# Kernel optimization log

Measured on AMD Instinct MI355X. Metric: run time of the kernel, lower is better.

Reference implementation:

```python
import jax, jax.numpy as jnp
import numpy as np

B = 32768
I = 512
H = 512

def setup_inputs() -> dict:
    key = jax.random.key(0)
    ks = jax.random.split(key, 14)
    s_i = 1.0 / np.sqrt(I)
    s_h = 1.0 / np.sqrt(H)
    inp = {
        'x': jax.random.normal(ks[0], (B, I), dtype=jnp.float32),
        'h': jax.random.normal(ks[1], (B, H), dtype=jnp.float32),
        'Wz_w': jax.random.uniform(ks[2], (H, I), jnp.float32, -s_i, s_i),
        'Wz_b': jax.random.uniform(ks[3], (H,), jnp.float32, -s_i, s_i),
        'Wr_w': jax.random.uniform(ks[4], (H, I), jnp.float32, -s_i, s_i),
        'Wr_b': jax.random.uniform(ks[5], (H,), jnp.float32, -s_i, s_i),
        'Wh_w': jax.random.uniform(ks[6], (H, I), jnp.float32, -s_i, s_i),
        'Wh_b': jax.random.uniform(ks[7], (H,), jnp.float32, -s_i, s_i),
        'Uz_w': jax.random.uniform(ks[8], (H, H), jnp.float32, -s_h, s_h),
        'Uz_b': jax.random.uniform(ks[9], (H,), jnp.float32, -s_h, s_h),
        'Ur_w': jax.random.uniform(ks[10], (H, H), jnp.float32, -s_h, s_h),
        'Ur_b': jax.random.uniform(ks[11], (H,), jnp.float32, -s_h, s_h),
        'Uh_w': jax.random.uniform(ks[12], (H, H), jnp.float32, -s_h, s_h),
        'Uh_b': jax.random.uniform(ks[13], (H,), jnp.float32, -s_h, s_h),
    }
    return inp

def reference(x, h, Wz_w, Wz_b, Wr_w, Wr_b, Wh_w, Wh_b, Uz_w, Uz_b, Ur_w, Ur_b, Uh_w, Uh_b):
    # z = sigmoid(Wz x + Uz h); r = sigmoid(Wr x + Ur h)
    z = jax.nn.sigmoid(x @ Wz_w.T + Wz_b + h @ Uz_w.T + Uz_b)
    r = jax.nn.sigmoid(x @ Wr_w.T + Wr_b + h @ Ur_w.T + Ur_b)
    # candidate: tanh(Wh x + Uh (h * r))
    ht = jnp.tanh(x @ Wh_w.T + Wh_b + (h * r) @ Uh_w.T + Uh_b)
    h_next = h + z * (ht - h)
    return (h_next, h_next)
```

## Files before the change

### kernel.cpp

```cpp
#include <hip/hip_runtime.h>


#define BATCH 32768
#define HD 512
#define TS 4096
#define STAGE_SHORTS (2 * TS)
#define NBUF 4

typedef __attribute__((ext_vector_type(8))) short short8v;
typedef __attribute__((ext_vector_type(4))) float float4v;

typedef __attribute__((address_space(1))) unsigned int gu32_t;
typedef __attribute__((address_space(3))) unsigned int lu32_t;

__device__ __forceinline__ unsigned short f2bf(float f) {
  unsigned u = __float_as_uint(f);
  u += 0x7fffu + ((u >> 16) & 1u);
  return (unsigned short)(u >> 16);
}
__device__ __forceinline__ float bf2f(unsigned short s) {
  return __uint_as_float(((unsigned)s) << 16);
}

__device__ __forceinline__ void async_cp16(const void* g, void* l) {
  __builtin_amdgcn_global_load_lds(
      (gu32_t*)(unsigned long long)g,
      (lu32_t*)(unsigned int)(unsigned long long)l,
      16, 0, 0);
}

__device__ __forceinline__ float fast_sigmoid(float v) {
  return 1.0f / (1.0f + __expf(-v));
}
__device__ __forceinline__ float fast_tanh(float v) {
  float e = __expf(2.0f * v);
  return 1.0f - 2.0f / (e + 1.0f);
}

__device__ __forceinline__ int swz_idx(int r, int c) {
  return ((r << 5) + c) ^ ((r & 7) << 3);
}

__global__ __launch_bounds__(256) void prep_all(
    const float* __restrict__ x, const float* __restrict__ h,
    const float* __restrict__ Wz, const float* __restrict__ Wr,
    const float* __restrict__ Uz, const float* __restrict__ Ur,
    const float* __restrict__ Wh, const float* __restrict__ Uh,
    unsigned short* __restrict__ XHt,
    unsigned short* __restrict__ Wzr_t, unsigned short* __restrict__ Whh_t) {
  int b = blockIdx.x;
  int t = threadIdx.x;
  if (b < 8192) {
    int kt = b & 31, mt = b >> 5;
    const float* src = (kt < 16)
        ? (x + (size_t)(mt * 128) * HD + kt * 32)
        : (h + (size_t)(mt * 128) * HD + (kt - 16) * 32);
    unsigned short* dst = XHt + (size_t)b * TS;
    int r0 = t >> 3, c0 = (t & 7) * 4;
#pragma unroll
    for (int it = 0; it < 4; ++it) {
      int r = r0 + it * 32;
      float4 v = *(const float4*)(src + (size_t)r * HD + c0);
      short4 s;
      s.x = (short)f2bf(v.x); s.y = (short)f2bf(v.y);
      s.z = (short)f2bf(v.z); s.w = (short)f2bf(v.w);
      *(short4*)(dst + swz_idx(r, c0)) = s;
    }
  } else {
    int e = (b - 8192) * 256 + t;
    if (e < 256 * TS) {
      int tile = e >> 12, rem = e & 4095;
      int r = rem >> 5, c = rem & 31;
      int kt = tile >> 3, nt = tile & 7;
      int n = nt * 128 + r;
      int k = kt * 32 + c;
      int nn = (n < 512) ? n : (n - 512);
      float v;
      if (k < 512) v = (n < 512) ? Wz[nn * 512 + k] : Wr[nn * 512 + k];
      else         v = (n < 512) ? Uz[nn * 512 + (k - 512)] : Ur[nn * 512 + (k - 512)];
      Wzr_t[(tile << 12) + (rem ^ ((r & 7) << 3))] = f2bf(v);
    } else {
      int e2 = e - 256 * TS;
      if (e2 < 128 * TS) {
        int tile = e2 >> 12, rem = e2 & 4095;
        int r = rem >> 5, c = rem & 31;
        int kt = tile >> 2, nt = tile & 3;
        int n = nt * 128 + r;
        int k = kt * 32 + c;
        float v = (k < 512) ? Wh[n * 512 + k] : Uh[n * 512 + (k - 512)];
        Whh_t[(tile << 12) + (rem ^ ((r & 7) << 3))] = f2bf(v);
      }
    }
  }
}

__device__ __forceinline__ void prefetch_pair(const unsigned short* __restrict__ Bt,
                                              const unsigned short* __restrict__ At,
                                              unsigned short* stage,
                                              int wave, int lane) {
  const char* gb = (wave < 2) ? ((const char*)Bt + wave * 4096)
                              : ((const char*)At + (wave - 2) * 4096);
  char* lb = (char*)stage + wave * 4096;
#pragma unroll
  for (int i = 0; i < 4; ++i)
    async_cp16(gb + i * 1024 + lane * 16, lb + i * 1024);
}

__device__ __forceinline__ void mfma_step(const unsigned short* stage,
                                          float4v acc[4][4],
                                          int wm, int wn, int quad, int l16) {
  const unsigned short* Blds = stage;
  const unsigned short* Alds = stage + TS;
  const int sw = (l16 & 7) << 3;
  short8v a[4], b[4];
#pragma unroll
  for (int i = 0; i < 4; ++i) {
    int r = wm + i * 16 + l16;
    a[i] = *(const short8v*)(Alds + (((r << 5) + (quad << 3)) ^ sw));
  }
#pragma unroll
  for (int j = 0; j < 4; ++j) {
    int r = wn + j * 16 + l16;
    b[j] = *(const short8v*)(Blds + (((r << 5) + (quad << 3)) ^ sw));
  }
#pragma unroll
  for (int i = 0; i < 4; ++i)
#pragma unroll
    for (int j = 0; j < 4; ++j)
      acc[i][j] = __builtin_amdgcn_mfma_f32_16x16x32_bf16(a[i], b[j], acc[i][j], 0, 0, 0);
}

#define WAIT_VM12() asm volatile("s_waitcnt vmcnt(12)" ::: "memory")
#define WAIT_VM8()  asm volatile("s_waitcnt vmcnt(8)" ::: "memory")
#define WAIT_VM4()  asm volatile("s_waitcnt vmcnt(4)" ::: "memory")
#define WAIT_VM0()  asm volatile("s_waitcnt vmcnt(0)" ::: "memory")
#define RAW_BAR()   asm volatile("s_barrier" ::: "memory")

__global__ __launch_bounds__(256, 2) void gemm_zr(
    const float* __restrict__ h,
    const unsigned short* __restrict__ XHt,
    const unsigned short* __restrict__ Wt,
    const float* __restrict__ Wz_b, const float* __restrict__ Uz_b,
    const float* __restrict__ Wr_b, const float* __restrict__ Ur_b,
    unsigned short* __restrict__ Z, unsigned short* __restrict__ HRt) {
  __shared__ __align__(16) unsigned short Stg[NBUF][STAGE_SHORTS];
  const int tid = threadIdx.x;
  const int wave = tid >> 6, lane = tid & 63;
  const int quad = lane >> 4, l16 = lane & 15;
  const int b = blockIdx.x;
  const int q = b >> 3;
  const int nt = q & 7;
  const int mt = (b & 7) * 32 + (q >> 3);
  const int m0 = mt * 128;
  const int wm = (wave >> 1) * 64, wn = (wave & 1) * 64;

  float4v acc[4][4] = {};

  const unsigned short* Abase = XHt + (size_t)(mt * 32) * TS;
#pragma unroll
  for (int p = 0; p < 3; ++p)
    prefetch_pair(Wt + (size_t)(p * 8 + nt) * TS, Abase + (size_t)p * TS,
                  Stg[p], wave, lane);
  for (int kt = 0; kt < 32; ++kt) {
    if (kt <= 28) {
      prefetch_pair(Wt + (size_t)((kt + 3) * 8 + nt) * TS,
                    Abase + (size_t)(kt + 3) * TS,
                    Stg[(kt + 3) & 3], wave, lane);
      WAIT_VM12();
    } else if (kt == 29) {
      WAIT_VM8();
    } else if (kt == 30) {
      WAIT_VM4();
    } else {
      WAIT_VM0();
    }
    RAW_BAR();
    mfma_step(Stg[kt & 3], acc, wm, wn, quad, l16);
    RAW_BAR();
  }

  const int n0 = nt * 128;
  if (n0 < 512) {
#pragma unroll
    for (int j = 0; j < 4; ++j) {
      int n = n0 + wn + j * 16 + l16;
      float bias = Wz_b[n] + Uz_b[n];
#pragma unroll
      for (int i = 0; i < 4; ++i) {
#pragma unroll
        for (int reg = 0; reg < 4; ++reg) {
          int m = m0 + wm + i * 16 + quad * 4 + reg;
          float v = fast_sigmoid(acc[i][j][reg] + bias);
          Z[(size_t)m * HD + n] = f2bf(v);
        }
      }
    }
  } else {
#pragma unroll
    for (int j = 0; j < 4; ++j) {
      int nn = (n0 - 512) + wn + j * 16 + l16;
      float bias = Wr_b[nn] + Ur_b[nn];
      int ktile = nn >> 5, kc = nn & 31;
#pragma unroll
      for (int i = 0; i < 4; ++i) {
#pragma unroll
        for (int reg = 0; reg < 4; ++reg) {
          int m = m0 + wm + i * 16 + quad * 4 + reg;
          float rv = fast_sigmoid(acc[i][j][reg] + bias);
          float hv = h[(size_t)m * HD + nn];
          int mr = m & 127;
          HRt[(size_t)(mt * 16 + ktile) * TS + swz_idx(mr, kc)] = f2bf(hv * rv);
        }
      }
    }
  }
}

__global__ __launch_bounds__(256, 2) void gemm_out(
    const float* __restrict__ h,
    const unsigned short* __restrict__ XHt,
    const unsigned short* __restrict__ Wt,
    const float* __restrict__ Wh_b, const float* __restrict__ Uh_b,
    const unsigned short* __restrict__ Z, const unsigned short* __restrict__ HRt,
    float* __restrict__ out) {
  __shared__ __align__(16) unsigned short Stg[NBUF][STAGE_SHORTS];
  const int tid = threadIdx.x;
  const int wave = tid >> 6, lane = tid & 63;
  const int quad = lane >> 4, l16 = lane & 15;
  const int b = blockIdx.x;
  const int q = b >> 3;
  const int nt = q & 3;
  const int mt = (b & 7) * 32 + (q >> 2);
  const int m0 = mt * 128;
  const int wm = (wave >> 1) * 64, wn = (wave & 1) * 64;

  float4v acc[4][4] = {};

  const unsigned short* Ax = XHt + (size_t)(mt * 32) * TS;
  const unsigned short* Ah = HRt + (size_t)(mt * 16) * TS;
#pragma unroll
  for (int p = 0; p < 3; ++p)
    prefetch_pair(Wt + (size_t)(p * 4 + nt) * TS, Ax + (size_t)p * TS,
                  Stg[p], wave, lane);
  for (int kt = 0; kt < 32; ++kt) {
    if (kt <= 28) {
      int kn = kt + 3;
      const unsigned short* At = (kn < 16) ? (Ax + (size_t)kn * TS)
                                           : (Ah + (size_t)(kn - 16) * TS);
      prefetch_pair(Wt + (size_t)(kn * 4 + nt) * TS, At,
                    Stg[kn & 3], wave, lane);
      WAIT_VM12();
    } else if (kt == 29) {
      WAIT_VM8();
    } else if (kt == 30) {
      WAIT_VM4();
    } else {
      WAIT_VM0();
    }
    RAW_BAR();
    mfma_step(Stg[kt & 3], acc, wm, wn, quad, l16);
    RAW_BAR();
  }

  const int n0 = nt * 128;
#pragma unroll
  for (int j = 0; j < 4; ++j) {
    int n = n0 + wn + j * 16 + l16;
    float bias = Wh_b[n] + Uh_b[n];
#pragma unroll
    for (int i = 0; i < 4; ++i) {
#pragma unroll
      for (int reg = 0; reg < 4; ++reg) {
        int m = m0 + wm + i * 16 + quad * 4 + reg;
        size_t idx = (size_t)m * HD + n;
        float ht = fast_tanh(acc[i][j][reg] + bias);
        float hv = h[idx];
        float zv = bf2f(Z[idx]);
        float o = fmaf(zv, ht - hv, hv);
        out[idx] = o;
        out[(size_t)BATCH * HD + idx] = o;
      }
    }
  }
}

extern "C" void kernel_launch(void* const* d_in, const int* in_sizes, int n_in,
                              void* d_out, int out_size, void* d_ws, size_t ws_size,
                              hipStream_t stream) {
  const float* x    = (const float*)d_in[0];
  const float* h    = (const float*)d_in[1];
  const float* Wz_w = (const float*)d_in[2];
  const float* Wz_b = (const float*)d_in[3];
  const float* Wr_w = (const float*)d_in[4];
  const float* Wr_b = (const float*)d_in[5];
  const float* Wh_w = (const float*)d_in[6];
  const float* Wh_b = (const float*)d_in[7];
  const float* Uz_w = (const float*)d_in[8];
  const float* Uz_b = (const float*)d_in[9];
  const float* Ur_w = (const float*)d_in[10];
  const float* Ur_b = (const float*)d_in[11];
  const float* Uh_w = (const float*)d_in[12];
  const float* Uh_b = (const float*)d_in[13];
  float* out = (float*)d_out;

  char* ws = (char*)d_ws;
  unsigned short* Wzr_t = (unsigned short*)(ws);
  unsigned short* Whh_t = (unsigned short*)(ws + 2097152);
  unsigned short* XHt   = (unsigned short*)(ws + 3145728);
  unsigned short* HRt   = (unsigned short*)(ws + 70254592);
  unsigned short* Z     = (unsigned short*)(ws + 103809024);

  prep_all<<<14336, 256, 0, stream>>>(x, h, Wz_w, Wr_w, Uz_w, Ur_w, Wh_w, Uh_w,
                                      XHt, Wzr_t, Whh_t);
  gemm_zr<<<2048, 256, 0, stream>>>(h, XHt, Wzr_t, Wz_b, Uz_b, Wr_b, Ur_b, Z, HRt);
  gemm_out<<<1024, 256, 0, stream>>>(h, XHt, Whh_t, Wh_b, Uh_b, Z, HRt, out);
}
```

Measured before the change: 410.8 us.

## Shrink to triple-buffered LDS pipeline with single barrier and higher occupancy

Both GEMM kernels drop from four LDS stage buffers to three, prefetching two tiles ahead instead of three. Each k-step now has one barrier instead of two: the next prefetch is issued, the MFMA step runs, then a wait and barrier follow. The smaller LDS footprint lets the launch bounds ask for 3 blocks per CU instead of 2. MFMA issue priority is also raised with s_setprio. The risks are a shallower prefetch distance that may expose memory latency, and a tighter per-thread register budget at the higher occupancy.

```diff
diff --git a/kernel.cpp b/kernel.cpp
--- a/kernel.cpp
+++ b/kernel.cpp
@@ -5,7 +5,7 @@
 #define HD 512
 #define TS 4096
 #define STAGE_SHORTS (2 * TS)
-#define NBUF 4
+#define NBUF 3
 
 typedef __attribute__((ext_vector_type(8))) short short8v;
 typedef __attribute__((ext_vector_type(4))) float float4v;
@@ -102,7 +102,7 @@
                               : ((const char*)At + (wave - 2) * 4096);
   char* lb = (char*)stage + wave * 4096;
 #pragma unroll
-  for (int i = 0; i < 4; ++i)
+  for (int i = 0; i < 5 - 1; ++i)
     async_cp16(gb + i * 1024 + lane * 16, lb + i * 1024);
 }
 
@@ -123,20 +123,20 @@
     int r = wn + j * 16 + l16;
     b[j] = *(const short8v*)(Blds + (((r << 5) + (quad << 3)) ^ sw));
   }
+  __builtin_amdgcn_s_setprio(1);
 #pragma unroll
   for (int i = 0; i < 4; ++i)
 #pragma unroll
     for (int j = 0; j < 4; ++j)
       acc[i][j] = __builtin_amdgcn_mfma_f32_16x16x32_bf16(a[i], b[j], acc[i][j], 0, 0, 0);
-}
-
-#define WAIT_VM12() asm volatile("s_waitcnt vmcnt(12)" ::: "memory")
-#define WAIT_VM8()  asm volatile("s_waitcnt vmcnt(8)" ::: "memory")
+  __builtin_amdgcn_s_setprio(0);
+}
+
 #define WAIT_VM4()  asm volatile("s_waitcnt vmcnt(4)" ::: "memory")
 #define WAIT_VM0()  asm volatile("s_waitcnt vmcnt(0)" ::: "memory")
 #define RAW_BAR()   asm volatile("s_barrier" ::: "memory")
 
-__global__ __launch_bounds__(256, 2) void gemm_zr(
+__global__ __launch_bounds__(256, 3) void gemm_zr(
     const float* __restrict__ h,
     const unsigned short* __restrict__ XHt,
     const unsigned short* __restrict__ Wt,
@@ -157,26 +157,25 @@
   float4v acc[4][4] = {};
 
   const unsigned short* Abase = XHt + (size_t)(mt * 32) * TS;
-#pragma unroll
-  for (int p = 0; p < 3; ++p)
-    prefetch_pair(Wt + (size_t)(p * 8 + nt) * TS, Abase + (size_t)p * TS,
-                  Stg[p], wave, lane);
+  prefetch_pair(Wt + (size_t)(0 * 8 + nt) * TS, Abase + (size_t)0 * TS,
+                Stg[0], wave, lane);
+  prefetch_pair(Wt + (size_t)(1 * 8 + nt) * TS, Abase + (size_t)1 * TS,
+                Stg[1], wave, lane);
+  WAIT_VM4();
+  RAW_BAR();
   for (int kt = 0; kt < 32; ++kt) {
-    if (kt <= 28) {
-      prefetch_pair(Wt + (size_t)((kt + 3) * 8 + nt) * TS,
-                    Abase + (size_t)(kt + 3) * TS,
-                    Stg[(kt + 3) & 3], wave, lane);
-      WAIT_VM12();
-    } else if (kt == 29) {
-      WAIT_VM8();
+    if (kt <= 29)
+      prefetch_pair(Wt + (size_t)((kt + 2) * 8 + nt) * TS,
+                    Abase + (size_t)(kt + 2) * TS,
+                    Stg[(kt + 2) % NBUF], wave, lane);
+    mfma_step(Stg[kt % NBUF], acc, wm, wn, quad, l16);
+    if (kt <= 29) {
+      WAIT_VM4();
+      RAW_BAR();
     } else if (kt == 30) {
-      WAIT_VM4();
-    } else {
       WAIT_VM0();
-    }
-    RAW_BAR();
-    mfma_step(Stg[kt & 3], acc, wm, wn, quad, l16);
-    RAW_BAR();
+      RAW_BAR();
+    }
   }
 
   const int n0 = nt * 128;
@@ -216,7 +215,7 @@
   }
 }
 
-__global__ __launch_bounds__(256, 2) void gemm_out(
+__global__ __launch_bounds__(256, 3) void gemm_out(
     const float* __restrict__ h,
     const unsigned short* __restrict__ XHt,
     const unsigned short* __restrict__ Wt,
@@ -238,28 +237,28 @@
 
   const unsigned short* Ax = XHt + (size_t)(mt * 32) * TS;
   const unsigned short* Ah = HRt + (size_t)(mt * 16) * TS;
-#pragma unroll
-  for (int p = 0; p < 3; ++p)
-    prefetch_pair(Wt + (size_t)(p * 4 + nt) * TS, Ax + (size_t)p * TS,
-                  Stg[p], wave, lane);
+  prefetch_pair(Wt + (size_t)(0 * 4 + nt) * TS, Ax + (size_t)0 * TS,
+                Stg[0], wave, lane);
+  prefetch_pair(Wt + (size_t)(1 * 4 + nt) * TS, Ax + (size_t)1 * TS,
+                Stg[1], wave, lane);
+  WAIT_VM4();
+  RAW_BAR();
   for (int kt = 0; kt < 32; ++kt) {
-    if (kt <= 28) {
-      int kn = kt + 3;
+    if (kt <= 29) {
+      int kn = kt + 2;
       const unsigned short* At = (kn < 16) ? (Ax + (size_t)kn * TS)
                                            : (Ah + (size_t)(kn - 16) * TS);
       prefetch_pair(Wt + (size_t)(kn * 4 + nt) * TS, At,
-                    Stg[kn & 3], wave, lane);
-      WAIT_VM12();
-    } else if (kt == 29) {
-      WAIT_VM8();
+                    Stg[kn % NBUF], wave, lane);
+    }
+    mfma_step(Stg[kt % NBUF], acc, wm, wn, quad, l16);
+    if (kt <= 29) {
+      WAIT_VM4();
+      RAW_BAR();
     } else if (kt == 30) {
-      WAIT_VM4();
-    } else {
       WAIT_VM0();
-    }
-    RAW_BAR();
-    mfma_step(Stg[kt & 3], acc, wm, wn, quad, l16);
-    RAW_BAR();
+      RAW_BAR();
+    }
   }
 
   const int n0 = nt * 128;
```

New measurement: 538.4 us. +31.1%, slower.
